# Kernel tuning notes

Hardware: AMD Instinct MI355X
Metric: run time of the kernel (lower is better)

## Reference

```python
import jax, jax.numpy as jnp
import numpy as np

B, N, INPUT, HIDDEN, WEIGHT = 1024, 50, 128, 256, 64
NEG_INF = -1.0e9


def setup_inputs() -> dict:
    key = jax.random.key(0)
    ks = jax.random.split(key, 12)
    s_in = 1.0 / np.sqrt(INPUT)
    s_h = 1.0 / np.sqrt(HIDDEN)
    s_w = 1.0 / np.sqrt(WEIGHT)
    return {
        "targets": jax.random.normal(ks[0], (B, N, INPUT), jnp.float32),
        "h0": jax.random.normal(ks[1], (B, HIDDEN), jnp.float32),
        "c0": jax.random.normal(ks[2], (B, HIDDEN), jnp.float32),
        # nn.Linear(input_size, hidden_size)
        "W_enc": jax.random.uniform(ks[3], (HIDDEN, INPUT), jnp.float32, -s_in, s_in),
        "b_enc": jax.random.uniform(ks[4], (HIDDEN,), jnp.float32, -s_in, s_in),
        # nn.LSTMCell(input_size, hidden_size)
        "W_ih": jax.random.uniform(ks[5], (4 * HIDDEN, INPUT), jnp.float32, -s_h, s_h),
        "W_hh": jax.random.uniform(ks[6], (4 * HIDDEN, HIDDEN), jnp.float32, -s_h, s_h),
        "b_ih": jax.random.uniform(ks[7], (4 * HIDDEN,), jnp.float32, -s_h, s_h),
        "b_hh": jax.random.uniform(ks[8], (4 * HIDDEN,), jnp.float32, -s_h, s_h),
        # W1, W2: Linear(hidden, weight, bias=False); vt: Linear(weight, 1, bias=False)
        "W1": jax.random.uniform(ks[9], (WEIGHT, HIDDEN), jnp.float32, -s_h, s_h),
        "W2": jax.random.uniform(ks[10], (WEIGHT, HIDDEN), jnp.float32, -s_h, s_h),
        "vt": jax.random.uniform(ks[11], (WEIGHT,), jnp.float32, -s_w, s_w),
    }


def _lstm_cell(x, h, c, W_ih, W_hh, b_ih, b_hh):
    gates = x @ W_ih.T + h @ W_hh.T + (b_ih + b_hh)  # [B, 4H]
    i, f, g, o = jnp.split(gates, 4, axis=-1)
    i, f, o = jax.nn.sigmoid(i), jax.nn.sigmoid(f), jax.nn.sigmoid(o)
    g = jnp.tanh(g)
    c_new = f * c + i * g
    h_new = o * jnp.tanh(c_new)
    return h_new, c_new


def _pointer_forward(targets, h0, c0, W_enc, b_enc, W_ih, W_hh, b_ih, b_hh, W1, W2, vt):
    b, n, _ = targets.shape
    encoder_states = targets @ W_enc.T + b_enc        # [B, N, H]
    blend1 = encoder_states @ W1.T                    # [B, N, W]
    col = jnp.arange(n)

    def step(carry, _):
        h, c, dec_in, selected = carry
        h, c = _lstm_cell(dec_in, h, c, W_ih, W_hh, b_ih, b_hh)
        blend2 = h @ W2.T                             # [B, W]
        out = jnp.tanh(blend1 + blend2[:, None, :]) @ vt  # [B, N]
        out = jnp.where(selected, NEG_INF, out)
        sel_idx = jnp.argmax(out, axis=-1)            # [B]
        selected = selected | (col[None, :] == sel_idx[:, None])
        p = jnp.maximum(jax.nn.softmax(out, axis=-1), 1e-9)
        dec_in = targets[jnp.arange(b), sel_idx]      # gather next input
        return (h, c, dec_in, selected), p

    dec_in0 = jnp.zeros_like(targets[:, 0])
    selected0 = jnp.zeros((b, n), dtype=bool)
    _, probs = jax.lax.scan(step, (h0, c0, dec_in0, selected0), None, length=n)
    return jnp.transpose(probs, (1, 0, 2))            # [B, N, N]


def reference(targets, h0, c0, W_enc, b_enc, W_ih, W_hh, b_ih, b_hh, W1, W2, vt):
    return _pointer_forward(targets, h0, c0, W_enc, b_enc, W_ih, W_hh, b_ih, b_hh, W1, W2, vt)
```

## Files before the change

### kernel.cpp

```cpp
#include <hip/hip_runtime.h>

#define O_WC     16
#define O_BC     (16 + 8192)
#define O_BIAS   (O_BC + 64)
#define O_BLEND1 16384
#define O_WB     3293184
#define O_XW     4194304
#define XW_FLOATS 52428800ULL
#define NEG_INF_V (-1.0e9f)

#define WB_TILE 12288
#define WB_W2   786432

using bf16x8 = __attribute__((ext_vector_type(8))) __bf16;
using f32x4  = __attribute__((ext_vector_type(4))) float;

__device__ __forceinline__ f32x4 mfma16(bf16x8 a, bf16x8 b, f32x4 c) {
  return __builtin_amdgcn_mfma_f32_16x16x32_bf16(a, b, c, 0, 0, 0);
}

__device__ __forceinline__ float b2f(unsigned int u) {
  union { unsigned int i; float f; } x; x.i = u << 16; return x.f;
}
__device__ __forceinline__ unsigned short f2b(float f) {
  union { float f; unsigned int i; } x; x.f = f;
  unsigned int r = x.i + 0x7fffu + ((x.i >> 16) & 1u);
  return (unsigned short)(r >> 16);
}
__device__ __forceinline__ float ldv(const void* p, int b16, long long i) {
  if (b16) return b2f(((const unsigned short*)p)[i]);
  return ((const float*)p)[i];
}
__device__ __forceinline__ float sigm(float x)  { return 1.0f / (1.0f + __expf(-x)); }
__device__ __forceinline__ float tanhx(float x) { return 1.0f - 2.0f / (1.0f + __expf(2.0f * x)); }

__device__ __forceinline__ float bfsel(const uint4& u, int e) {
  unsigned int w = (e < 2) ? u.x : (e < 4) ? u.y : (e < 6) ? u.z : u.w;
  union { unsigned int i; float f; } x;
  x.i = (e & 1) ? (w & 0xffff0000u) : (w << 16);
  return x.f;
}

__global__ __launch_bounds__(256) void prepAll(
    const void* b_enc, const void* b_ih, const void* b_hh, const void* W1,
    const void* W_ih, const void* W_hh, const void* W2, float* ws) {
  __shared__ int anybig;
  const int t = threadIdx.x;
  const int blk = blockIdx.x;
  if (t == 0) anybig = 0;
  __syncthreads();
  {
    unsigned short u = ((const unsigned short*)b_enc)[t];
    float f = b2f((unsigned int)u);
    if (!(fabsf(f) <= 1.0f)) atomicOr(&anybig, 1);
  }
  __syncthreads();
  const int b16 = anybig ? 0 : 1;

  if (blk == 0) {
    if (t == 0) ((int*)ws)[0] = b16;
    for (int k = t; k < 1024; k += 256)
      ws[O_BIAS + k] = ldv(b_ih, b16, k) + ldv(b_hh, b16, k);
    if (t < 64) {
      float acc = 0.f;
      for (int h = 0; h < 256; ++h)
        acc += ldv(W1, b16, t * 256 + h) * ldv(b_enc, b16, h);
      ws[O_BC + t] = acc;
    }
  }
  unsigned short* wb = (unsigned short*)(ws + O_WB);
  const int i = blk * 256 + t;
  {
    int g = i >> 8, k = i & 255;
    int nt = g >> 4, r = g & 15;
    int kc = k >> 5, lane = ((k >> 3) & 3) * 16 + r, e = k & 7;
    float w = ldv(W_hh, b16, i);
    unsigned short hi = f2b(w);
    long long d = (long long)nt * WB_TILE + kc * 512 + lane * 8 + e;
    wb[d] = hi;
    wb[d + 4096] = f2b(w - b2f((unsigned int)hi));
  }
  if (i < 131072) {
    int g = i >> 7, k = i & 127;
    int nt = g >> 4, r = g & 15;
    int kc = k >> 5, lane = ((k >> 3) & 3) * 16 + r, e = k & 7;
    float w = ldv(W_ih, b16, i);
    unsigned short hi = f2b(w);
    long long d = (long long)nt * WB_TILE + 8192 + kc * 512 + lane * 8 + e;
    wb[d] = hi;
    wb[d + 2048] = f2b(w - b2f((unsigned int)hi));
  }
  if (i < 16384) {
    int g = i >> 8, k = i & 255;
    int ntw = g >> 4, r = g & 15;
    int kc = k >> 5, lane = ((k >> 3) & 3) * 16 + r, e = k & 7;
    float w = ldv(W2, b16, i);
    unsigned short hi = f2b(w);
    long long d = WB_W2 + ntw * 8192 + kc * 512 + lane * 8 + e;
    wb[d] = hi;
    wb[d + 4096] = f2b(w - b2f((unsigned int)hi));
  }
}

__global__ void prep1(const void* W_enc, const void* W1, const void* b_enc,
                      float* ws) {
  __shared__ int anybig;
  int t = threadIdx.x;
  if (t == 0) anybig = 0;
  __syncthreads();
  {
    unsigned short u = ((const unsigned short*)b_enc)[t];
    float f = b2f((unsigned int)u);
    if (!(fabsf(f) <= 1.0f)) atomicOr(&anybig, 1);
  }
  __syncthreads();
  int b16 = anybig ? 0 : 1;
  int o = blockIdx.x * 256 + t;
  int w = o >> 7, i = o & 127;
  float acc = 0.f;
  for (int h = 0; h < 256; ++h)
    acc += ldv(W1, b16, w * 256 + h) * ldv(W_enc, b16, h * 128 + i);
  ws[O_WC + o] = acc;
}

__global__ __launch_bounds__(256) void blendk(const void* targets, float* ws) {
  __shared__ float tg[6400];
  __shared__ float wc[8192];
  int b16 = ((const int*)ws)[0];
  int t = threadIdx.x, b = blockIdx.x;
  for (int k = t; k < 8192; k += 256) wc[k] = ws[O_WC + k];
  if (b16) {
    const unsigned short* tp = (const unsigned short*)targets + (long long)b * 6400;
    for (int k = t * 8; k < 6400; k += 2048) {
      uint4 u = *(const uint4*)(tp + k);
      #pragma unroll
      for (int e = 0; e < 8; ++e) tg[k + e] = bfsel(u, e);
    }
  } else {
    const float* tp = (const float*)targets + (long long)b * 6400;
    for (int k = t; k < 6400; k += 256) tg[k] = tp[k];
  }
  __syncthreads();
  int w = t & 63, j0 = t >> 6;
  float bcv = ws[O_BC + w];
  for (int j = j0; j < 50; j += 4) {
    float acc = 0.f;
    for (int i0 = 0; i0 < 128; i0 += 8) {
      const float4* q = (const float4*)(wc + w * 128 + i0);
      float4 a = q[0], bb = q[1];
      const float* x = &tg[j * 128 + i0];
      acc += a.x * x[0] + a.y * x[1] + a.z * x[2] + a.w * x[3]
           + bb.x * x[4] + bb.y * x[5] + bb.z * x[6] + bb.w * x[7];
    }
    ws[O_BLEND1 + (b * 50 + j) * 64 + w] = acc + bcv;
  }
}

__global__ __launch_bounds__(512)
__attribute__((amdgpu_waves_per_eu(2, 2)))
void xwK(const void* targets, float* ws) {
  __shared__ __align__(16) unsigned short tgS[4][32][264];
  const int b16 = ((const int*)ws)[0];
  const int t = threadIdx.x;
  const int b0 = blockIdx.x * 4;
  const unsigned short* wb = (const unsigned short*)(ws + O_WB);
  float* xwp = ws + O_XW;
  const int l = t & 63, Wv = t >> 6, lr = l & 15, hc = l >> 4;

  #pragma unroll 1
  for (int half = 0; half < 2; ++half) {
    __syncthreads();
    for (int k = t; k < 4 * 32 * 128; k += 512) {
      int p = k >> 12, jr = (k >> 7) & 31, i = k & 127;
      int j = half * 32 + jr;
      float v = (j < 50) ? ldv(targets, b16, ((long long)(b0 + p) * 50 + j) * 128 + i)
                         : 0.f;
      unsigned short hi = f2b(v);
      tgS[p][jr][i]       = hi;
      tgS[p][jr][128 + i] = f2b(v - b2f((unsigned int)hi));
    }
    __syncthreads();
    const int njg = (half == 0) ? 4 : 3;
    #pragma unroll 1
    for (int ti = 0; ti < 8; ++ti) {
      const int nt = Wv * 8 + ti;
      const unsigned short* tb = wb + (long long)nt * WB_TILE + 8192 + l * 8;
      bf16x8 wih[8];
      #pragma unroll
      for (int kc = 0; kc < 4; ++kc) {
        wih[kc]     = *(const bf16x8*)(tb + kc * 512);
        wih[4 + kc] = *(const bf16x8*)(tb + 2048 + kc * 512);
      }
      #pragma unroll 1
      for (int p = 0; p < 4; ++p) {
        #pragma unroll 1
        for (int jh = 0; jh < njg; ++jh) {
          bf16x8 ax[4];
          const unsigned short* tp =
              &tgS[p][jh * 8 + (lr & 7)][((lr < 8) ? 0 : 128) + hc * 8];
          #pragma unroll
          for (int kc = 0; kc < 4; ++kc) ax[kc] = *(const bf16x8*)(tp + kc * 32);
          f32x4 cH = {0.f,0.f,0.f,0.f}, cL = {0.f,0.f,0.f,0.f};
          #pragma unroll
          for (int kc = 0; kc < 4; ++kc) {
            cH = mfma16(ax[kc], wih[kc], cH);
            cL = mfma16(ax[kc], wih[4 + kc], cL);
          }
          f32x4 acc = cH + cL;
          float s0 = acc[0] + __shfl_xor(acc[0], 32, 64);
          float s1 = acc[1] + __shfl_xor(acc[1], 32, 64);
          float s2 = acc[2] + __shfl_xor(acc[2], 32, 64);
          float s3 = acc[3] + __shfl_xor(acc[3], 32, 64);
          if (l < 32) {
            int jb = half * 32 + jh * 8 + hc * 4;
            long long ro = (long long)(b0 + p) * 50;
            if (jb + 0 < 50) xwp[(ro + jb + 0) * 1024 + nt * 16 + lr] = s0;
            if (jb + 1 < 50) xwp[(ro + jb + 1) * 1024 + nt * 16 + lr] = s1;
            if (jb + 2 < 50) xwp[(ro + jb + 2) * 1024 + nt * 16 + lr] = s2;
            if (jb + 3 < 50) xwp[(ro + jb + 3) * 1024 + nt * 16 + lr] = s3;
          }
        }
      }
    }
  }
}

__global__ __launch_bounds__(1024)
__attribute__((amdgpu_waves_per_eu(4, 4)))
void mainX(const void* targets, const void* h0, const void* c0, const void* vt,
           float* ws, void* outp) {
  __shared__ __align__(16) unsigned short hS[16][264];
  __shared__ __align__(16) float xwS[4][1024];
  __shared__ float bl1S[4][50][66];
  __shared__ float cT[4][256];
  __shared__ float gsh[4][1024];
  __shared__ float bias_s[1024];
  __shared__ float b2s[4][64];
  __shared__ float vt_s[64];
  __shared__ int   selidx[4];
  __shared__ int   selb[4][64];
  __shared__ int   auxcnt;

  const int b16 = ((const int*)ws)[0];
  const int t = threadIdx.x;
  const int bbase = blockIdx.x * 4;
  const unsigned short* wb = (const unsigned short*)(ws + O_WB);
  const float* xw = ws + O_XW;

  bias_s[t] = ws[O_BIAS + t];
  if (t < 64) vt_s[t] = ldv(vt, b16, t);
  if (t < 256) selb[t >> 6][t & 63] = 0;
  if (t < 4) selidx[t] = -1;
  if (t == 0) auxcnt = 0;
  {
    unsigned short* z1 = &hS[0][0];
    for (int k = t; k < 16 * 264; k += 1024) z1[k] = 0;
  }
  for (int k = t; k < 12800; k += 1024) {
    int p = k / 3200, r = k - p * 3200, j = r >> 6, w = r & 63;
    bl1S[p][j][w] = ws[O_BLEND1 + (((long long)(bbase + p) * 50 + j) << 6) + w];
  }
  __syncthreads();
  {
    int p = t >> 8, j = t & 255;
    float h = ldv(h0, b16, (long long)(bbase + p) * 256 + j);
    float c = ldv(c0, b16, (long long)(bbase + p) * 256 + j);
    unsigned short hi = f2b(h);
    hS[p][j]     = hi;
    hS[p + 4][j] = f2b(h - b2f((unsigned int)hi));
    cT[p][j]     = c;
  }
  __syncthreads();

  const int l  = t & 63, Wv = t >> 6;
  const int lr = l & 15, hc = l >> 4;

  {
    bf16x8 ah[8];
    #pragma unroll
    for (int kc = 0; kc < 8; ++kc)
      ah[kc] = *(const bf16x8*)&hS[lr][kc * 32 + hc * 8];
    #pragma unroll 1
    for (int nt = Wv; nt < 64; nt += 16) {
      const unsigned short* tb = wb + (long long)nt * WB_TILE + l * 8;
      bf16x8 wh[4], wl[4];
      #pragma unroll
      for (int q2 = 0; q2 < 4; ++q2) {
        wh[q2] = *(const bf16x8*)(tb + q2 * 512);
        wl[q2] = *(const bf16x8*)(tb + 4096 + q2 * 512);
      }
      f32x4 aH = {0.f,0.f,0.f,0.f}, aL = {0.f,0.f,0.f,0.f};
      #pragma unroll
      for (int kc = 0; kc < 8; ++kc) {
        const int cur = kc & 3;
        aH = mfma16(ah[kc], wh[cur], aH);
        aL = mfma16(ah[kc], wl[cur], aL);
        if (kc + 4 < 8) {
          wh[cur] = *(const bf16x8*)(tb + (kc + 4) * 512);
          wl[cur] = *(const bf16x8*)(tb + 4096 + (kc + 4) * 512);
        }
      }
      f32x4 acc = aH + aL;
      float s0 = acc[0] + __shfl_xor(acc[0], 16, 64);
      float s1 = acc[1] + __shfl_xor(acc[1], 16, 64);
      float s2 = acc[2] + __shfl_xor(acc[2], 16, 64);
      float s3 = acc[3] + __shfl_xor(acc[3], 16, 64);
      if (l < 16) {
        const int g = nt * 16 + l;
        gsh[0][g] = s0; gsh[1][g] = s1; gsh[2][g] = s2; gsh[3][g] = s3;
      }
    }
  }
  __syncthreads();

  #pragma unroll 1
  for (int step = 0; step < 50; ++step) {
    {
      int j = t & 255, p = t >> 8;
      float gi = gsh[p][j], gf = gsh[p][256 + j];
      float gg = gsh[p][512 + j], go = gsh[p][768 + j];
      if (selidx[p] >= 0) {
        gi += xwS[p][j]; gf += xwS[p][256 + j];
        gg += xwS[p][512 + j]; go += xwS[p][768 + j];
      }
      gi = sigm (gi + bias_s[j]);
      gf = sigm (gf + bias_s[256 + j]);
      gg = tanhx(gg + bias_s[512 + j]);
      go = sigm (go + bias_s[768 + j]);
      float c = gf * cT[p][j] + gi * gg;
      cT[p][j] = c;
      float h = go * tanhx(c);
      unsigned short hi = f2b(h);
      hS[p][j]     = hi;
      hS[p + 4][j] = f2b(h - b2f((unsigned int)hi));
    }
    __syncthreads();

    if (Wv >= 4) {
      if (step < 49) {
        bf16x8 ah[8];
        #pragma unroll
        for (int kc = 0; kc < 8; ++kc)
          ah[kc] = *(const bf16x8*)&hS[lr][kc * 32 + hc * 8];
        #pragma unroll 1
        for (int nt = Wv - 4; nt < 64; nt += 12) {
          const unsigned short* tb = wb + (long long)nt * WB_TILE + l * 8;
          bf16x8 wh[4], wl[4];
          #pragma unroll
          for (int q2 = 0; q2 < 4; ++q2) {
            wh[q2] = *(const bf16x8*)(tb + q2 * 512);
            wl[q2] = *(const bf16x8*)(tb + 4096 + q2 * 512);
          }
          f32x4 aH = {0.f,0.f,0.f,0.f}, aL = {0.f,0.f,0.f,0.f};
          #pragma unroll
          for (int kc = 0; kc < 8; ++kc) {
            const int cur = kc & 3;
            aH = mfma16(ah[kc], wh[cur], aH);
            aL = mfma16(ah[kc], wl[cur], aL);
            if (kc + 4 < 8) {
              wh[cur] = *(const bf16x8*)(tb + (kc + 4) * 512);
              wl[cur] = *(const bf16x8*)(tb + 4096 + (kc + 4) * 512);
            }
          }
          f32x4 acc = aH + aL;
          float s0 = acc[0] + __shfl_xor(acc[0], 16, 64);
          float s1 = acc[1] + __shfl_xor(acc[1], 16, 64);
          float s2 = acc[2] + __shfl_xor(acc[2], 16, 64);
          float s3 = acc[3] + __shfl_xor(acc[3], 16, 64);
          if (l < 16) {
            const int g = nt * 16 + l;
            gsh[0][g] = s0; gsh[1][g] = s1; gsh[2][g] = s2; gsh[3][g] = s3;
          }
        }
      }
    } else {
      {
        bf16x8 bh[8];
        #pragma unroll
        for (int kc = 0; kc < 8; ++kc)
          bh[kc] = *(const bf16x8*)&hS[lr][kc * 32 + hc * 8];
        const unsigned short* tb2 = wb + WB_W2 + Wv * 8192 + l * 8;
        f32x4 cH = {0.f,0.f,0.f,0.f}, cL = {0.f,0.f,0.f,0.f};
        #pragma unroll
        for (int kc = 0; kc < 8; ++kc) {
          cH = mfma16(bh[kc], *(const bf16x8*)(tb2 + kc * 512), cH);
          cL = mfma16(bh[kc], *(const bf16x8*)(tb2 + 4096 + kc * 512), cL);
        }
        f32x4 acc = cH + cL;
        float s0 = acc[0] + __shfl_xor(acc[0], 16, 64);
        float s1 = acc[1] + __shfl_xor(acc[1], 16, 64);
        float s2 = acc[2] + __shfl_xor(acc[2], 16, 64);
        float s3 = acc[3] + __shfl_xor(acc[3], 16, 64);
        if (l < 16) {
          const int g = Wv * 16 + l;
          b2s[0][g] = s0; b2s[1][g] = s1; b2s[2][g] = s2; b2s[3][g] = s3;
        }
      }
      __threadfence_block();
      if (l == 0)
        __hip_atomic_fetch_add(&auxcnt, 1, __ATOMIC_RELEASE,
                               __HIP_MEMORY_SCOPE_WORKGROUP);
      while (__hip_atomic_load(&auxcnt, __ATOMIC_ACQUIRE,
                               __HIP_MEMORY_SCOPE_WORKGROUP) < 4 * (step + 1))
        __builtin_amdgcn_s_sleep(2);

      {
        const int p = Wv, lane = l;
        float outv = -3.4e38f;
        if (lane < 50) {
          float acc = 0.f;
          #pragma unroll 8
          for (int w = 0; w < 64; ++w)
            acc += vt_s[w] * tanhx(bl1S[p][lane][w] + b2s[p][w]);
          outv = selb[p][lane] ? NEG_INF_V : acc;
        }
        float v = outv;
        int idx = lane;
        #pragma unroll
        for (int msk = 1; msk < 64; msk <<= 1) {
          float ov = __shfl_xor(v, msk, 64);
          int   oi = __shfl_xor(idx, msk, 64);
          if (ov > v || (ov == v && oi < idx)) { v = ov; idx = oi; }
        }
        {
          const float* xr = xw + ((long long)(bbase + p) * 50 + idx) * 1024;
          #pragma unroll
          for (int kk = 0; kk < 4; ++kk)
            *(float4*)&xwS[p][lane * 4 + kk * 256] =
                *(const float4*)(xr + lane * 4 + kk * 256);
        }
        float e = (lane < 50) ? __expf(outv - v) : 0.f;
        float ssum = e;
        #pragma unroll
        for (int msk = 1; msk < 64; msk <<= 1) ssum += __shfl_xor(ssum, msk, 64);
        if (lane < 50) {
          float prob = fmaxf(e / ssum, 1e-9f);
          long long o = (long long)(bbase + p) * 2500 + step * 50 + lane;
          if (b16) ((unsigned short*)outp)[o] = f2b(prob);
          else     ((float*)outp)[o] = prob;
        }
        if (lane == 0) selidx[p] = idx;
        if (lane == idx) selb[p][idx] = 1;
      }
    }
    __syncthreads();
  }
}

__global__ __launch_bounds__(512)
__attribute__((amdgpu_waves_per_eu(2, 2)))
void mainK6(const void* targets, const void* h0, const void* c0, const void* vt,
            float* ws, void* outp) {
  __shared__ __align__(16) unsigned short hS[16][264];
  __shared__ __align__(16) unsigned short xA[16][136];
  __shared__ float cT[8][256];
  __shared__ float gsh[8][1024];
  __shared__ float bias_s[1024];
  __shared__ float b2s[8][64];
  __shared__ float outs[8][64];
  __shared__ float vt_s[64];
  __shared__ int   selidx[8];
  __shared__ int   selb[8][64];

  const int b16 = ((const int*)ws)[0];
  const int t = threadIdx.x;
  const int bbase = blockIdx.x * 8;
  const unsigned short* wb = (const unsigned short*)(ws + O_WB);

  for (int k = t; k < 1024; k += 512) bias_s[k] = ws[O_BIAS + k];
  if (t < 64) vt_s[t] = ldv(vt, b16, t);
  if (t < 512) selb[t >> 6][t & 63] = 0;
  if (t < 8) selidx[t] = -1;
  {
    unsigned short* z1 = &hS[0][0];
    unsigned short* z2 = &xA[0][0];
    for (int k = t; k < 16 * 264; k += 512) z1[k] = 0;
    for (int k = t; k < 16 * 136; k += 512) z2[k] = 0;
  }
  __syncthreads();
  for (int k = t; k < 2048; k += 512) {
    int p = k >> 8, j = k & 255;
    float h = ldv(h0, b16, (long long)(bbase + p) * 256 + j);
    float c = ldv(c0, b16, (long long)(bbase + p) * 256 + j);
    unsigned short hi = f2b(h);
    hS[p][j]     = hi;
    hS[p + 8][j] = f2b(h - b2f((unsigned int)hi));
    cT[p][j]     = c;
  }
  __syncthreads();

  const int l  = t & 63, Wv = t >> 6;
  const int lr = l & 15;

  #pragma unroll 1
  for (int step = 0; step < 50; ++step) {
    {
      bf16x8 ah[8], ax[4];
      #pragma unroll
      for (int kc = 0; kc < 8; ++kc)
        ah[kc] = *(const bf16x8*)&hS[lr][kc * 32 + (l >> 4) * 8];
      #pragma unroll
      for (int kc = 0; kc < 4; ++kc)
        ax[kc] = *(const bf16x8*)&xA[lr][kc * 32 + (l >> 4) * 8];
      #pragma unroll 1
      for (int ti = 0; ti < 8; ++ti) {
        const int nt = Wv * 8 + ti;
        const unsigned short* tb = wb + (long long)nt * WB_TILE + l * 8;
        bf16x8 wH[12], wL[12];
        #pragma unroll
        for (int kc = 0; kc < 8; ++kc) {
          wH[kc] = *(const bf16x8*)(tb + kc * 512);
          wL[kc] = *(const bf16x8*)(tb + 4096 + kc * 512);
        }
        #pragma unroll
        for (int kc = 0; kc < 4; ++kc) {
          wH[8 + kc] = *(const bf16x8*)(tb + 8192 + kc * 512);
          wL[8 + kc] = *(const bf16x8*)(tb + 10240 + kc * 512);
        }
        f32x4 aH = {0.f,0.f,0.f,0.f}, aL = {0.f,0.f,0.f,0.f};
        #pragma unroll
        for (int kc = 0; kc < 8; ++kc) {
          aH = mfma16(ah[kc], wH[kc], aH);
          aL = mfma16(ah[kc], wL[kc], aL);
        }
        #pragma unroll
        for (int kc = 0; kc < 4; ++kc) {
          aH = mfma16(ax[kc], wH[8 + kc], aH);
          aL = mfma16(ax[kc], wL[8 + kc], aL);
        }
        f32x4 acc = aH + aL;
        float s0 = acc[0] + __shfl_xor(acc[0], 32, 64);
        float s1 = acc[1] + __shfl_xor(acc[1], 32, 64);
        float s2 = acc[2] + __shfl_xor(acc[2], 32, 64);
        float s3 = acc[3] + __shfl_xor(acc[3], 32, 64);
        if (l < 32) {
          const int g = nt * 16 + (l & 15), pb = (l >> 4) * 4;
          gsh[pb + 0][g] = s0; gsh[pb + 1][g] = s1;
          gsh[pb + 2][g] = s2; gsh[pb + 3][g] = s3;
        }
      }
    }
    __syncthreads();

    for (int k = t; k < 2048; k += 512) {
      int j = k & 255, p = k >> 8;
      float gi = sigm (gsh[p][j]       + bias_s[j]);
      float gf = sigm (gsh[p][256 + j] + bias_s[256 + j]);
      float gg = tanhx(gsh[p][512 + j] + bias_s[512 + j]);
      float go = sigm (gsh[p][768 + j] + bias_s[768 + j]);
      float c = gf * cT[p][j] + gi * gg;
      cT[p][j] = c;
      float h = go * tanhx(c);
      unsigned short hi = f2b(h);
      hS[p][j]     = hi;
      hS[p + 8][j] = f2b(h - b2f((unsigned int)hi));
    }
    __syncthreads();

    if (Wv < 4) {
      bf16x8 bh[8];
      #pragma unroll
      for (int kc = 0; kc < 8; ++kc)
        bh[kc] = *(const bf16x8*)&hS[lr][kc * 32 + (l >> 4) * 8];
      const unsigned short* tb = wb + WB_W2 + Wv * 8192 + l * 8;
      f32x4 aH = {0.f,0.f,0.f,0.f}, aL = {0.f,0.f,0.f,0.f};
      #pragma unroll
      for (int kc = 0; kc < 8; ++kc) {
        aH = mfma16(bh[kc], *(const bf16x8*)(tb + kc * 512), aH);
        aL = mfma16(bh[kc], *(const bf16x8*)(tb + 4096 + kc * 512), aL);
      }
      f32x4 acc = aH + aL;
      float s0 = acc[0] + __shfl_xor(acc[0], 32, 64);
      float s1 = acc[1] + __shfl_xor(acc[1], 32, 64);
      float s2 = acc[2] + __shfl_xor(acc[2], 32, 64);
      float s3 = acc[3] + __shfl_xor(acc[3], 32, 64);
      if (l < 32) {
        const int g = Wv * 16 + (l & 15), pb = (l >> 4) * 4;
        b2s[pb + 0][g] = s0; b2s[pb + 1][g] = s1;
        b2s[pb + 2][g] = s2; b2s[pb + 3][g] = s3;
      }
    }
    __syncthreads();

    if (t < 400) {
      int p = t / 50, j = t - p * 50;
      const float* bl = ws + O_BLEND1 + (((bbase + p) * 50 + j) * 64);
      float acc = 0.f;
      #pragma unroll
      for (int v4 = 0; v4 < 16; ++v4) {
        float4 bv = *(const float4*)(bl + v4 * 4);
        int w0 = v4 * 4;
        acc += vt_s[w0 + 0] * tanhx(bv.x + b2s[p][w0 + 0]);
        acc += vt_s[w0 + 1] * tanhx(bv.y + b2s[p][w0 + 1]);
        acc += vt_s[w0 + 2] * tanhx(bv.z + b2s[p][w0 + 2]);
        acc += vt_s[w0 + 3] * tanhx(bv.w + b2s[p][w0 + 3]);
      }
      outs[p][j] = selb[p][j] ? NEG_INF_V : acc;
    }
    __syncthreads();

    {
      int p = Wv, lane = l;
      float v = (lane < 50) ? outs[p][lane] : -3.4e38f;
      int idx = lane;
      #pragma unroll
      for (int msk = 1; msk < 64; msk <<= 1) {
        float ov = __shfl_xor(v, msk, 64);
        int   oi = __shfl_xor(idx, msk, 64);
        if (ov > v || (ov == v && oi < idx)) { v = ov; idx = oi; }
      }
      float e = (lane < 50) ? __expf(outs[p][lane] - v) : 0.f;
      float ssum = e;
      #pragma unroll
      for (int msk = 1; msk < 64; msk <<= 1) ssum += __shfl_xor(ssum, msk, 64);
      if (lane < 50) {
        float prob = fmaxf(e / ssum, 1e-9f);
        int o = (bbase + p) * 2500 + step * 50 + lane;
        if (b16) ((unsigned short*)outp)[o] = f2b(prob);
        else     ((float*)outp)[o] = prob;
      }
      if (lane == 0) selidx[p] = idx;
      if (lane == idx) selb[p][idx] = 1;
    }
    __syncthreads();

    for (int k = t; k < 1024; k += 512) {
      int p = k >> 7, i = k & 127;
      float xf = ldv(targets, b16,
                     ((long long)(bbase + p) * 50 + selidx[p]) * 128 + i);
      unsigned short hi = f2b(xf);
      xA[p][i]     = hi;
      xA[p + 8][i] = f2b(xf - b2f((unsigned int)hi));
    }
    __syncthreads();
  }
}

extern "C" void kernel_launch(void* const* d_in, const int* in_sizes, int n_in,
                              void* d_out, int out_size, void* d_ws, size_t ws_size,
                              hipStream_t stream) {
  (void)in_sizes; (void)n_in; (void)out_size;
  const void* targets = d_in[0];
  const void* h0      = d_in[1];
  const void* c0      = d_in[2];
  const void* W_enc   = d_in[3];
  const void* b_enc   = d_in[4];
  const void* W_ih    = d_in[5];
  const void* W_hh    = d_in[6];
  const void* b_ih    = d_in[7];
  const void* b_hh    = d_in[8];
  const void* W1      = d_in[9];
  const void* W2      = d_in[10];
  const void* vt      = d_in[11];
  float* ws = (float*)d_ws;

  int use_xw = (ws_size >= ((size_t)O_XW + (size_t)XW_FLOATS) * 4) ? 1 : 0;

  prepAll<<<1024, 256, 0, stream>>>(b_enc, b_ih, b_hh, W1, W_ih, W_hh, W2, ws);
  prep1<<<32, 256, 0, stream>>>(W_enc, W1, b_enc, ws);
  blendk<<<1024, 256, 0, stream>>>(targets, ws);
  if (use_xw) {
    xwK<<<256, 512, 0, stream>>>(targets, ws);
    mainX<<<256, 1024, 0, stream>>>(targets, h0, c0, vt, ws, d_out);
  } else {
    mainK6<<<128, 512, 0, stream>>>(targets, h0, c0, vt, ws, d_out);
  }
}
```

Baseline: 856.1 us.

## Merge prep1 into prepAll and rebalance recurrent MFMA tiles across waves

Folds the W1·W_enc precompute kernel into extra blocks of prepAll, removing one kernel launch. In the main recurrent kernel, the 64 W_hh gate tiles are no longer strided across 12 waves (uneven 5 or 6 tiles each). Instead each of 12 waves takes 5 contiguous tiles, and the last 4 tiles are computed by the attention/softmax waves after their pointer work, balancing per-step load. This adds extra register use and work on the attention waves, which could lengthen their critical path.

New measurement: 833.3 us. 1.03x faster.

```diff
diff --git a/kernel.cpp b/kernel.cpp
--- a/kernel.cpp
+++ b/kernel.cpp
@@ -43,7 +43,8 @@
 
 __global__ __launch_bounds__(256) void prepAll(
     const void* b_enc, const void* b_ih, const void* b_hh, const void* W1,
-    const void* W_ih, const void* W_hh, const void* W2, float* ws) {
+    const void* W_ih, const void* W_hh, const void* W2, const void* W_enc,
+    float* ws) {
   __shared__ int anybig;
   const int t = threadIdx.x;
   const int blk = blockIdx.x;
@@ -56,6 +57,16 @@
   }
   __syncthreads();
   const int b16 = anybig ? 0 : 1;
+
+  if (blk >= 1024) {
+    int o = (blk - 1024) * 256 + t;
+    int w = o >> 7, ii = o & 127;
+    float acc = 0.f;
+    for (int h = 0; h < 256; ++h)
+      acc += ldv(W1, b16, w * 256 + h) * ldv(W_enc, b16, h * 128 + ii);
+    ws[O_WC + o] = acc;
+    return;
+  }
 
   if (blk == 0) {
     if (t == 0) ((int*)ws)[0] = b16;
@@ -100,27 +111,6 @@
     wb[d] = hi;
     wb[d + 4096] = f2b(w - b2f((unsigned int)hi));
   }
-}
-
-__global__ void prep1(const void* W_enc, const void* W1, const void* b_enc,
-                      float* ws) {
-  __shared__ int anybig;
-  int t = threadIdx.x;
-  if (t == 0) anybig = 0;
-  __syncthreads();
-  {
-    unsigned short u = ((const unsigned short*)b_enc)[t];
-    float f = b2f((unsigned int)u);
-    if (!(fabsf(f) <= 1.0f)) atomicOr(&anybig, 1);
-  }
-  __syncthreads();
-  int b16 = anybig ? 0 : 1;
-  int o = blockIdx.x * 256 + t;
-  int w = o >> 7, i = o & 127;
-  float acc = 0.f;
-  for (int h = 0; h < 256; ++h)
-    acc += ldv(W1, b16, w * 256 + h) * ldv(W_enc, b16, h * 128 + i);
-  ws[O_WC + o] = acc;
 }
 
 __global__ __launch_bounds__(256) void blendk(const void* targets, float* ws) {
@@ -342,8 +332,10 @@
         #pragma unroll
         for (int kc = 0; kc < 8; ++kc)
           ah[kc] = *(const bf16x8*)&hS[lr][kc * 32 + hc * 8];
+        const int nt0 = (Wv - 4) * 5;
         #pragma unroll 1
-        for (int nt = Wv - 4; nt < 64; nt += 12) {
+        for (int k5 = 0; k5 < 5; ++k5) {
+          const int nt = nt0 + k5;
           const unsigned short* tb = wb + (long long)nt * WB_TILE + l * 8;
           bf16x8 wh[4], wl[4];
           #pragma unroll
@@ -442,6 +434,40 @@
         if (lane == 0) selidx[p] = idx;
         if (lane == idx) selb[p][idx] = 1;
       }
+      if (step < 49) {
+        bf16x8 ah[8];
+        #pragma unroll
+        for (int kc = 0; kc < 8; ++kc)
+          ah[kc] = *(const bf16x8*)&hS[lr][kc * 32 + hc * 8];
+        const int nt = 60 + Wv;
+        const unsigned short* tb = wb + (long long)nt * WB_TILE + l * 8;
+        bf16x8 wh[4], wl[4];
+        #pragma unroll
+        for (int q2 = 0; q2 < 4; ++q2) {
+          wh[q2] = *(const bf16x8*)(tb + q2 * 512);
+          wl[q2] = *(const bf16x8*)(tb + 4096 + q2 * 512);
+        }
+        f32x4 aH = {0.f,0.f,0.f,0.f}, aL = {0.f,0.f,0.f,0.f};
+        #pragma unroll
+        for (int kc = 0; kc < 8; ++kc) {
+          const int cur = kc & 3;
+          aH = mfma16(ah[kc], wh[cur], aH);
+          aL = mfma16(ah[kc], wl[cur], aL);
+          if (kc + 4 < 8) {
+            wh[cur] = *(const bf16x8*)(tb + (kc + 4) * 512);
+            wl[cur] = *(const bf16x8*)(tb + 4096 + (kc + 4) * 512);
+          }
+        }
+        f32x4 acc = aH + aL;
+        float s0 = acc[0] + __shfl_xor(acc[0], 16, 64);
+        float s1 = acc[1] + __shfl_xor(acc[1], 16, 64);
+        float s2 = acc[2] + __shfl_xor(acc[2], 16, 64);
+        float s3 = acc[3] + __shfl_xor(acc[3], 16, 64);
+        if (l < 16) {
+          const int g = nt * 16 + l;
+          gsh[0][g] = s0; gsh[1][g] = s1; gsh[2][g] = s2; gsh[3][g] = s3;
+        }
+      }
     }
     __syncthreads();
   }
@@ -656,8 +682,8 @@
 
   int use_xw = (ws_size >= ((size_t)O_XW + (size_t)XW_FLOATS) * 4) ? 1 : 0;
 
-  prepAll<<<1024, 256, 0, stream>>>(b_enc, b_ih, b_hh, W1, W_ih, W_hh, W2, ws);
-  prep1<<<32, 256, 0, stream>>>(W_enc, W1, b_enc, ws);
+  prepAll<<<1056, 256, 0, stream>>>(b_enc, b_ih, b_hh, W1, W_ih, W_hh, W2,
+                                    W_enc, ws);
   blendk<<<1024, 256, 0, stream>>>(targets, ws);
   if (use_xw) {
     xwK<<<256, 512, 0, stream>>>(targets, ws);
```
